# Kernel optimization log

Hardware: AMD Instinct MI355X
Metric: run time of the kernel (lower is better)

Reference implementation:

```python
import jax, jax.numpy as jnp
import numpy as np

N = 100000      # nodes
E = 3200000     # edges (avg degree 32)
F_IN = 128      # data.num_features
H = 64          # hidden_channels
L = 64          # num_layers
C = 47          # data.num_classes
ALPHA = 0.1
THETA = 0.5


def setup_inputs() -> dict:
    key = jax.random.key(0)
    ks = jax.random.split(key, 8)
    x = jax.random.normal(ks[0], (N, F_IN), dtype=jnp.float32)
    edge_index = jax.random.randint(ks[1], (2, E), 0, N, dtype=jnp.int64)
    # Linear(F_IN, H), Linear(H, C), and L shared GCN2Conv weights [H, H]
    W1 = jax.random.normal(ks[2], (F_IN, H), dtype=jnp.float32) * 0.05
    b1 = jnp.zeros((H,), dtype=jnp.float32)
    conv_W = jax.random.normal(ks[3], (L, H, H), dtype=jnp.float32) * 0.05
    W2 = jax.random.normal(ks[4], (H, C), dtype=jnp.float32) * 0.05
    b2 = jnp.zeros((C,), dtype=jnp.float32)
    return {"x": x, "edge_index": edge_index, "W1": W1, "b1": b1,
            "conv_W": conv_W, "W2": W2, "b2": b2}


def reference(x, edge_index, W1, b1, conv_W, W2, b2):
    # --- normalized adjacency with renormalization trick: D^-1/2 (A + I) D^-1/2, transposed ---
    sl = jnp.arange(N, dtype=edge_index.dtype)
    r = jnp.concatenate([edge_index[1], sl])  # adj_t rows (destinations)
    c = jnp.concatenate([edge_index[0], sl])  # adj_t cols (sources)
    deg = jax.ops.segment_sum(jnp.ones((r.shape[0],), jnp.float32), r, num_segments=N)
    dinv = jax.lax.rsqrt(deg)                 # self-loops guarantee deg >= 1
    w = dinv[r] * dinv[c]                     # [E + N] edge weights

    def spmm(h):  # A_hat @ h via gather + segment scatter-add
        return jax.ops.segment_sum(w[:, None] * h[c], r, num_segments=N)

    # dropout is identity in eval mode
    x0 = jax.nn.relu(x @ W1 + b1)             # [N, H]
    betas = jnp.log(THETA / jnp.arange(1, L + 1, dtype=jnp.float32) + 1.0)

    def step(h, layer):
        Wl, beta = layer
        p = spmm(h)
        s = (1.0 - ALPHA) * p + ALPHA * x0    # initial-residual mix
        h = jax.nn.relu((1.0 - beta) * s + beta * (s @ Wl))  # identity mapping
        return h, None

    h, _ = jax.lax.scan(step, x0, (conv_W, betas))
    logits = h @ W2 + b2                      # [N, C]
    return jax.nn.log_softmax(logits, axis=-1)
```

## Files before the change

### kernel.cpp

```cpp
#include <hip/hip_runtime.h>
#include <hip/hip_bf16.h>
#include <math.h>

#define NN 100000
#define NE 3200000
#define FIN 128
#define HD 64
#define NL 64
#define NC 47
#define RPW 4
#define WPB 4
#define RPB (RPW * WPB)

#define SEGSH 13
#define NSEG 13
#define NKEY (NN * NSEG)
#define KB ((NKEY + 1023) / 1024)


__device__ __forceinline__ float bf2f(unsigned short u) {
    union { unsigned int i; float f; } v; v.i = ((unsigned int)u) << 16; return v.f;
}
__device__ __forceinline__ unsigned short f2bf(float f) {
    __hip_bfloat16 h = __float2bfloat16(f);
    return *reinterpret_cast<unsigned short*>(&h);
}
__device__ __forceinline__ float bflo(unsigned int u) {
    union { unsigned int i; float f; } v; v.i = u << 16; return v.f;
}
__device__ __forceinline__ float bfhi(unsigned int u) {
    union { unsigned int i; float f; } v; v.i = u & 0xFFFF0000u; return v.f;
}
__device__ __forceinline__ float fin_at(const void* p, int isf32, size_t i) {
    return isf32 ? ((const float*)p)[i]
                 : __bfloat162float(((const __hip_bfloat16*)p)[i]);
}
__device__ __forceinline__ int edge_at(const void* p, int is64, size_t i) {
    return is64 ? (int)((const long long*)p)[i] : ((const int*)p)[i];
}


__global__ void detect_kernel(const void* __restrict__ x, const void* __restrict__ eidx,
                              int* __restrict__ flags) {
    if (threadIdx.x == 0 && blockIdx.x == 0) {
        const unsigned short* u = (const unsigned short*)x;
        int sane = 0;
        for (int i = 0; i < 64; i++) {
            unsigned short v = u[2 * i];
            int e = (v >> 7) & 0xFF;
            if ((v & 0x7FFF) == 0 || (e >= 90 && e <= 141)) sane++;
        }
        flags[0] = (sane >= 48) ? 0 : 1;
        const int* e32 = (const int*)eidx;
        int nz = 0;
        for (int i = 0; i < 64; i++) if (e32[2 * i + 1] != 0) nz++;
        flags[1] = (nz == 0) ? 1 : 0;
    }
}


__global__ void key_count(const void* __restrict__ eidx, const int* __restrict__ flags,
                          int* __restrict__ cnt) {
    int e = blockIdx.x * blockDim.x + threadIdx.x;
    if (e < NE) {
        int is64 = flags[1];
        int s = edge_at(eidx, is64, (size_t)e);
        int d = edge_at(eidx, is64, (size_t)NE + e);
        atomicAdd(&cnt[d * NSEG + (s >> SEGSH)], 1);
    }
}

__global__ __launch_bounds__(1024) void scan_reduce(const int* __restrict__ cnt,
                                                    int* __restrict__ bsum) {
    __shared__ int lds[1024];
    int tid = threadIdx.x;
    int i = blockIdx.x * 1024 + tid;
    lds[tid] = (i < NKEY) ? cnt[i] : 0;
    __syncthreads();
    for (int off = 512; off > 0; off >>= 1) {
        if (tid < off) lds[tid] += lds[tid + off];
        __syncthreads();
    }
    if (tid == 0) bsum[blockIdx.x] = lds[0];
}

__global__ __launch_bounds__(1024) void scan_mid(int* __restrict__ bsum, int* __restrict__ total_out) {
    __shared__ int lds[1024];
    __shared__ int base_s;
    int tid = threadIdx.x;
    if (tid == 0) base_s = 0;
    __syncthreads();
    for (int chunk = 0; chunk < KB; chunk += 1024) {
        int i = chunk + tid;
        int v = (i < KB) ? bsum[i] : 0;
        lds[tid] = v;
        __syncthreads();
        for (int off = 1; off < 1024; off <<= 1) {
            int t = (tid >= off) ? lds[tid - off] : 0;
            __syncthreads();
            lds[tid] += t;
            __syncthreads();
        }
        int incl = lds[tid];
        int base = base_s;
        if (i < KB) bsum[i] = base + incl - v;
        __syncthreads();
        if (tid == 1023) base_s = base + incl;
        __syncthreads();
    }
    if (tid == 0) *total_out = base_s;
}

__global__ __launch_bounds__(1024) void scan_final(const int* __restrict__ cnt,
                                                   const int* __restrict__ bsum,
                                                   int* __restrict__ keyptr) {
    __shared__ int lds[1024];
    int tid = threadIdx.x;
    int i = blockIdx.x * 1024 + tid;
    int v = (i < NKEY) ? cnt[i] : 0;
    lds[tid] = v;
    __syncthreads();
    for (int off = 1; off < 1024; off <<= 1) {
        int t = (tid >= off) ? lds[tid - off] : 0;
        __syncthreads();
        lds[tid] += t;
        __syncthreads();
    }
    if (i < NKEY) keyptr[i] = bsum[blockIdx.x] + lds[tid] - v;
}

__global__ void dinv_kernel(const int* __restrict__ keyptr, float* __restrict__ dinv) {
    int i = blockIdx.x * blockDim.x + threadIdx.x;
    if (i < NN) {
        int deg = keyptr[(i + 1) * NSEG] - keyptr[i * NSEG];
        dinv[i] = rsqrtf(1.0f + (float)deg);
    }
}

__global__ void scatter_kernel(const void* __restrict__ eidx, const int* __restrict__ flags,
                               const int* __restrict__ keyptr, int* __restrict__ fill,
                               int* __restrict__ col) {
    int e = blockIdx.x * blockDim.x + threadIdx.x;
    if (e < NE) {
        int is64 = flags[1];
        int s = edge_at(eidx, is64, (size_t)e);
        int d = edge_at(eidx, is64, (size_t)NE + e);
        int key = d * NSEG + (s >> SEGSH);
        int pos = keyptr[key] + atomicAdd(&fill[key], 1);
        col[pos] = s;
    }
}


__global__ __launch_bounds__(256) void x0_kernel(const void* __restrict__ x,
                                                 const void* __restrict__ W1,
                                                 const void* __restrict__ b1,
                                                 const int* __restrict__ flags,
                                                 const float* __restrict__ dinv,
                                                 unsigned short* __restrict__ x0b,
                                                 unsigned short* __restrict__ g0) {
    __shared__ float lw[FIN * HD];
    int isf = flags[0];
    int tid = threadIdx.x;
    for (int i = tid; i < FIN * HD; i += 256) lw[i] = fin_at(W1, isf, i);
    __syncthreads();
    int wave = tid >> 6, lane = tid & 63;
    int row0 = blockIdx.x * RPB + wave * RPW;
    if (row0 >= NN) return;
    unsigned int pa01, pa23, pb01, pb23;
    {
        unsigned short a0 = f2bf(fin_at(x, isf, (size_t)(row0 + 0) * FIN + lane));
        unsigned short a1 = f2bf(fin_at(x, isf, (size_t)(row0 + 1) * FIN + lane));
        unsigned short a2 = f2bf(fin_at(x, isf, (size_t)(row0 + 2) * FIN + lane));
        unsigned short a3 = f2bf(fin_at(x, isf, (size_t)(row0 + 3) * FIN + lane));
        unsigned short c0 = f2bf(fin_at(x, isf, (size_t)(row0 + 0) * FIN + 64 + lane));
        unsigned short c1 = f2bf(fin_at(x, isf, (size_t)(row0 + 1) * FIN + 64 + lane));
        unsigned short c2 = f2bf(fin_at(x, isf, (size_t)(row0 + 2) * FIN + 64 + lane));
        unsigned short c3 = f2bf(fin_at(x, isf, (size_t)(row0 + 3) * FIN + 64 + lane));
        pa01 = ((unsigned int)a0 << 16) | a1;  pa23 = ((unsigned int)a2 << 16) | a3;
        pb01 = ((unsigned int)c0 << 16) | c1;  pb23 = ((unsigned int)c2 << 16) | c3;
    }
    float bias = fin_at(b1, isf, lane);
    float d0 = bias, d1 = bias, d2 = bias, d3 = bias;
    #pragma unroll 8
    for (int k = 0; k < 64; k++) {
        float w = lw[k * HD + lane];
        unsigned int b01 = __shfl(pa01, k, 64);
        unsigned int b23 = __shfl(pa23, k, 64);
        union { unsigned int i; float f; } f0, f1, f2, f3;
        f0.i = b01 & 0xFFFF0000u; f1.i = b01 << 16;
        f2.i = b23 & 0xFFFF0000u; f3.i = b23 << 16;
        d0 += f0.f * w; d1 += f1.f * w; d2 += f2.f * w; d3 += f3.f * w;
    }
    #pragma unroll 8
    for (int k = 0; k < 64; k++) {
        float w = lw[(64 + k) * HD + lane];
        unsigned int b01 = __shfl(pb01, k, 64);
        unsigned int b23 = __shfl(pb23, k, 64);
        union { unsigned int i; float f; } f0, f1, f2, f3;
        f0.i = b01 & 0xFFFF0000u; f1.i = b01 << 16;
        f2.i = b23 & 0xFFFF0000u; f3.i = b23 << 16;
        d0 += f0.f * w; d1 += f1.f * w; d2 += f2.f * w; d3 += f3.f * w;
    }
    float dd[RPW] = {d0, d1, d2, d3};
    #pragma unroll
    for (int r = 0; r < RPW; r++) {
        int row = row0 + r;
        if (row >= NN) continue;
        float v = fmaxf(dd[r], 0.0f);
        x0b[(size_t)row * HD + lane] = f2bf(v);
        g0[(size_t)row * HD + lane] = f2bf(dinv[row] * v);
    }
}


__global__ __launch_bounds__(256, 8) void layer_fused(const int* __restrict__ keyptr,
                                                      const int* __restrict__ col,
                                                      const float* __restrict__ dinv,
                                                      const unsigned short* __restrict__ g_in,
                                                      const unsigned short* __restrict__ x0b,
                                                      unsigned short* __restrict__ g_out,
                                                      const void* __restrict__ convW, int layer,
                                                      const int* __restrict__ flags, float beta) {
    __shared__ float lw[HD * HD];
    int isf = flags[0];
    size_t wbase = (size_t)layer * HD * HD;
    int tid = threadIdx.x;
    for (int i = tid; i < HD * HD; i += 256) lw[i] = fin_at(convW, isf, wbase + i);
    __syncthreads();

    int wave = __builtin_amdgcn_readfirstlane(tid >> 6);
    int lane = tid & 63;
    int eslot = lane >> 3;
    int sbyte = (lane & 7) << 4;
    const char* gb = (const char*)g_in;

    int row0 = blockIdx.x * RPB + wave * RPW;

    float sacc[RPW];
    float dsc[RPW];
    #pragma unroll
    for (int r = 0; r < RPW; r++) {
        int row = row0 + r;
        if (row >= NN) { sacc[r] = 0.0f; dsc[r] = 1.0f; continue; }
        int start = keyptr[row * NSEG];
        int end   = keyptr[(row + 1) * NSEG];

        float a0 = 0.0f, a1 = 0.0f, a2 = 0.0f, a3 = 0.0f;
        float a4 = 0.0f, a5 = 0.0f, a6 = 0.0f, a7 = 0.0f;

        for (int j = start; j < end; j += 32) {
            int le = end - 1;
            int i0 = j + eslot, i1 = i0 + 8, i2 = i0 + 16, i3 = i0 + 24;
            int c0 = col[i0 < end ? i0 : le];
            int c1 = col[i1 < end ? i1 : le];
            int c2 = col[i2 < end ? i2 : le];
            int c3 = col[i3 < end ? i3 : le];
            uint4 u0 = *reinterpret_cast<const uint4*>(gb + (((size_t)c0) << 7) + sbyte);
            uint4 u1 = *reinterpret_cast<const uint4*>(gb + (((size_t)c1) << 7) + sbyte);
            uint4 u2 = *reinterpret_cast<const uint4*>(gb + (((size_t)c2) << 7) + sbyte);
            uint4 u3 = *reinterpret_cast<const uint4*>(gb + (((size_t)c3) << 7) + sbyte);
            float m0 = (i0 < end) ? 1.0f : 0.0f;
            float m1 = (i1 < end) ? 1.0f : 0.0f;
            float m2 = (i2 < end) ? 1.0f : 0.0f;
            float m3 = (i3 < end) ? 1.0f : 0.0f;
            a0 = fmaf(m0, bflo(u0.x), a0); a1 = fmaf(m0, bfhi(u0.x), a1);
            a2 = fmaf(m0, bflo(u0.y), a2); a3 = fmaf(m0, bfhi(u0.y), a3);
            a4 = fmaf(m0, bflo(u0.z), a4); a5 = fmaf(m0, bfhi(u0.z), a5);
            a6 = fmaf(m0, bflo(u0.w), a6); a7 = fmaf(m0, bfhi(u0.w), a7);
            a0 = fmaf(m1, bflo(u1.x), a0); a1 = fmaf(m1, bfhi(u1.x), a1);
            a2 = fmaf(m1, bflo(u1.y), a2); a3 = fmaf(m1, bfhi(u1.y), a3);
            a4 = fmaf(m1, bflo(u1.z), a4); a5 = fmaf(m1, bfhi(u1.z), a5);
            a6 = fmaf(m1, bflo(u1.w), a6); a7 = fmaf(m1, bfhi(u1.w), a7);
            a0 = fmaf(m2, bflo(u2.x), a0); a1 = fmaf(m2, bfhi(u2.x), a1);
            a2 = fmaf(m2, bflo(u2.y), a2); a3 = fmaf(m2, bfhi(u2.y), a3);
            a4 = fmaf(m2, bflo(u2.z), a4); a5 = fmaf(m2, bfhi(u2.z), a5);
            a6 = fmaf(m2, bflo(u2.w), a6); a7 = fmaf(m2, bfhi(u2.w), a7);
            a0 = fmaf(m3, bflo(u3.x), a0); a1 = fmaf(m3, bfhi(u3.x), a1);
            a2 = fmaf(m3, bflo(u3.y), a2); a3 = fmaf(m3, bfhi(u3.y), a3);
            a4 = fmaf(m3, bflo(u3.z), a4); a5 = fmaf(m3, bfhi(u3.z), a5);
            a6 = fmaf(m3, bflo(u3.w), a6); a7 = fmaf(m3, bfhi(u3.w), a7);
        }

        a0 += __shfl_xor(a0, 8, 64); a0 += __shfl_xor(a0, 16, 64); a0 += __shfl_xor(a0, 32, 64);
        a1 += __shfl_xor(a1, 8, 64); a1 += __shfl_xor(a1, 16, 64); a1 += __shfl_xor(a1, 32, 64);
        a2 += __shfl_xor(a2, 8, 64); a2 += __shfl_xor(a2, 16, 64); a2 += __shfl_xor(a2, 32, 64);
        a3 += __shfl_xor(a3, 8, 64); a3 += __shfl_xor(a3, 16, 64); a3 += __shfl_xor(a3, 32, 64);
        a4 += __shfl_xor(a4, 8, 64); a4 += __shfl_xor(a4, 16, 64); a4 += __shfl_xor(a4, 32, 64);
        a5 += __shfl_xor(a5, 8, 64); a5 += __shfl_xor(a5, 16, 64); a5 += __shfl_xor(a5, 32, 64);
        a6 += __shfl_xor(a6, 8, 64); a6 += __shfl_xor(a6, 16, 64); a6 += __shfl_xor(a6, 32, 64);
        a7 += __shfl_xor(a7, 8, 64); a7 += __shfl_xor(a7, 16, 64); a7 += __shfl_xor(a7, 32, 64);

        int srcl = lane >> 3;
        float t0 = __shfl(a0, srcl, 64);
        float t1 = __shfl(a1, srcl, 64);
        float t2 = __shfl(a2, srcl, 64);
        float t3 = __shfl(a3, srcl, 64);
        float t4 = __shfl(a4, srcl, 64);
        float t5 = __shfl(a5, srcl, 64);
        float t6 = __shfl(a6, srcl, 64);
        float t7 = __shfl(a7, srcl, 64);
        int b0 = lane & 1, b1 = (lane >> 1) & 1, b2 = (lane >> 2) & 1;
        float s01 = b0 ? t1 : t0, s23 = b0 ? t3 : t2;
        float s45 = b0 ? t5 : t4, s67 = b0 ? t7 : t6;
        float sA = b1 ? s23 : s01, sB = b1 ? s67 : s45;
        float gsum = b2 ? sB : sA;

        float a = gsum + bf2f(g_in[((size_t)row << 6) + lane]);
        float di = dinv[row];
        dsc[r] = di;
        sacc[r] = 0.9f * (di * a) + 0.1f * bf2f(x0b[((size_t)row << 6) + lane]);
    }

    unsigned int p01 = ((unsigned int)f2bf(sacc[0]) << 16) | f2bf(sacc[1]);
    unsigned int p23 = ((unsigned int)f2bf(sacc[2]) << 16) | f2bf(sacc[3]);
    float d0 = 0.0f, d1 = 0.0f, d2 = 0.0f, d3 = 0.0f;
    #pragma unroll 8
    for (int k = 0; k < 64; k++) {
        float w = lw[k * HD + lane];
        unsigned int b01 = __shfl(p01, k, 64);
        unsigned int b23 = __shfl(p23, k, 64);
        union { unsigned int i; float f; } f0, f1, f2, f3;
        f0.i = b01 & 0xFFFF0000u; f1.i = b01 << 16;
        f2.i = b23 & 0xFFFF0000u; f3.i = b23 << 16;
        d0 += f0.f * w; d1 += f1.f * w;
        d2 += f2.f * w; d3 += f3.f * w;
    }

    float dd[RPW] = {d0, d1, d2, d3};
    float omb = 1.0f - beta;
    #pragma unroll
    for (int r = 0; r < RPW; r++) {
        int row = row0 + r;
        if (row >= NN) continue;
        float res = omb * sacc[r] + beta * dd[r];
        g_out[((size_t)row << 6) + lane] = f2bf(dsc[r] * fmaxf(res, 0.0f));
    }
}


__global__ __launch_bounds__(256) void out_kernel(const unsigned short* __restrict__ g,
                                                  const float* __restrict__ dinv,
                                                  const void* __restrict__ W2,
                                                  const void* __restrict__ b2,
                                                  const int* __restrict__ flags,
                                                  void* __restrict__ out) {
    __shared__ float lw[HD * 64];
    int isf = flags[0];
    int tid = threadIdx.x;
    for (int i = tid; i < HD * 64; i += 256) {
        int k = i >> 6, j = i & 63;
        lw[i] = (j < NC) ? fin_at(W2, isf, (size_t)k * NC + j) : 0.0f;
    }
    __syncthreads();
    int row = blockIdx.x * 4 + (tid >> 6);
    int lane = tid & 63;
    if (row >= NN) return;
    float hv = bf2f(g[(size_t)row * HD + lane]) / dinv[row];
    float acc = (lane < NC) ? fin_at(b2, isf, lane) : 0.0f;
    #pragma unroll 8
    for (int k = 0; k < 64; k++) {
        float hk = __shfl(hv, k, 64);
        acc += hk * lw[k * 64 + lane];
    }
    float mv = (lane < NC) ? acc : -1e30f;
    for (int off = 32; off > 0; off >>= 1) mv = fmaxf(mv, __shfl_xor(mv, off, 64));
    float ex = (lane < NC) ? expf(acc - mv) : 0.0f;
    float se = ex;
    for (int off = 32; off > 0; off >>= 1) se += __shfl_xor(se, off, 64);
    float res = acc - mv - logf(se);
    if (lane < NC) {
        size_t oi = (size_t)row * NC + lane;
        if (isf) ((float*)out)[oi] = res;
        else     ((__hip_bfloat16*)out)[oi] = __float2bfloat16(res);
    }
}


static inline size_t align256(size_t x) { return (x + 255) & ~(size_t)255; }

extern "C" void kernel_launch(void* const* d_in, const int* in_sizes, int n_in,
                              void* d_out, int out_size, void* d_ws, size_t ws_size,
                              hipStream_t stream) {
    const void* x     = d_in[0];
    const void* eidx  = d_in[1];
    const void* W1    = d_in[2];
    const void* b1    = d_in[3];
    const void* convW = d_in[4];
    const void* W2    = d_in[5];
    const void* b2    = d_in[6];

    char* p = (char*)d_ws;
    size_t off = 0;
    auto alloc = [&](size_t bytes) { void* r = p + off; off += align256(bytes); return r; };
    int*            flags   = (int*)alloc(256);
    int*            cnt     = (int*)alloc((size_t)NKEY * 4);
    int*            fill    = (int*)alloc((size_t)NKEY * 4);
    int*            keyptr  = (int*)alloc((size_t)(NKEY + 1) * 4);
    int*            bsum    = (int*)alloc((size_t)KB * 4);
    float*          dinv    = (float*)alloc((size_t)NN * 4);
    int*            col     = (int*)alloc((size_t)NE * 4);
    unsigned short* x0b     = (unsigned short*)alloc((size_t)NN * HD * 2);
    unsigned short* hA      = (unsigned short*)alloc((size_t)NN * HD * 2);
    unsigned short* hB      = (unsigned short*)alloc((size_t)NN * HD * 2);

    detect_kernel<<<1, 64, 0, stream>>>(x, eidx, flags);

    hipMemsetAsync(cnt, 0, (size_t)NKEY * 4, stream);
    hipMemsetAsync(fill, 0, (size_t)NKEY * 4, stream);
    key_count<<<(NE + 255) / 256, 256, 0, stream>>>(eidx, flags, cnt);
    scan_reduce<<<KB, 1024, 0, stream>>>(cnt, bsum);
    scan_mid<<<1, 1024, 0, stream>>>(bsum, keyptr + NKEY);
    scan_final<<<KB, 1024, 0, stream>>>(cnt, bsum, keyptr);
    dinv_kernel<<<(NN + 255) / 256, 256, 0, stream>>>(keyptr, dinv);
    scatter_kernel<<<(NE + 255) / 256, 256, 0, stream>>>(eidx, flags, keyptr, fill, col);

    int fb = (NN + RPB - 1) / RPB;
    x0_kernel<<<fb, 256, 0, stream>>>(x, W1, b1, flags, dinv, x0b, hA);

    unsigned short* gin = hA;
    unsigned short* gout = hB;
    for (int l = 0; l < NL; l++) {
        float beta = logf(0.5f / (float)(l + 1) + 1.0f);
        layer_fused<<<fb, 256, 0, stream>>>(keyptr, col, dinv, gin, x0b, gout,
                                            convW, l, flags, beta);
        unsigned short* t = gin; gin = gout; gout = t;
    }
    out_kernel<<<(NN + 3) / 4, 256, 0, stream>>>(gin, dinv, W2, b2, flags, (void*)d_out);
}
```

Baseline: 6.611 ms.

## Split SpMM into source-quadrant partial sums plus separate combine kernel

Edges are now bucketed by source index modulo 4, replacing the old 13-segment source-range bucketing, and each layer runs as two kernels. The first computes per-quadrant partial sums into a float workspace using 8-lane groups that each gather one 128-byte row. The second sums the partials, applies the residual mix and the 64x64 weight matmul. The aim is more parallelism and a different gather pattern, at the cost of writing and reading a 4x N x 64 fp32 buffer every layer plus an extra launch per layer. The old fused path remains as a fallback when the workspace is too small.

```diff
diff --git a/kernel.cpp b/kernel.cpp
--- a/kernel.cpp
+++ b/kernel.cpp
@@ -12,10 +12,12 @@
 #define WPB 4
 #define RPB (RPW * WPB)
 
-#define SEGSH 13
-#define NSEG 13
-#define NKEY (NN * NSEG)
+#define NQ 4
+#define NSEG 4
+#define NKEY (NN * NQ)
 #define KB ((NKEY + 1023) / 1024)
+
+typedef float f32x4 __attribute__((ext_vector_type(4)));
 
 
 __device__ __forceinline__ float bf2f(unsigned short u) {
@@ -60,13 +62,15 @@
 
 
 __global__ void key_count(const void* __restrict__ eidx, const int* __restrict__ flags,
-                          int* __restrict__ cnt) {
+                          int* __restrict__ cnt, int big) {
     int e = blockIdx.x * blockDim.x + threadIdx.x;
     if (e < NE) {
         int is64 = flags[1];
         int s = edge_at(eidx, is64, (size_t)e);
         int d = edge_at(eidx, is64, (size_t)NE + e);
-        atomicAdd(&cnt[d * NSEG + (s >> SEGSH)], 1);
+        int q = s & 3;
+        int key = big ? (q * NN + d) : (d * 4 + q);
+        atomicAdd(&cnt[key], 1);
     }
 }
 
@@ -129,23 +133,32 @@
     if (i < NKEY) keyptr[i] = bsum[blockIdx.x] + lds[tid] - v;
 }
 
-__global__ void dinv_kernel(const int* __restrict__ keyptr, float* __restrict__ dinv) {
+__global__ void dinv_kernel(const int* __restrict__ keyptr, float* __restrict__ dinv, int big) {
     int i = blockIdx.x * blockDim.x + threadIdx.x;
     if (i < NN) {
-        int deg = keyptr[(i + 1) * NSEG] - keyptr[i * NSEG];
+        int deg;
+        if (big) {
+            deg = 0;
+            #pragma unroll
+            for (int q = 0; q < NQ; q++)
+                deg += keyptr[q * NN + i + 1] - keyptr[q * NN + i];
+        } else {
+            deg = keyptr[(i + 1) * NSEG] - keyptr[i * NSEG];
+        }
         dinv[i] = rsqrtf(1.0f + (float)deg);
     }
 }
 
 __global__ void scatter_kernel(const void* __restrict__ eidx, const int* __restrict__ flags,
                                const int* __restrict__ keyptr, int* __restrict__ fill,
-                               int* __restrict__ col) {
+                               int* __restrict__ col, int big) {
     int e = blockIdx.x * blockDim.x + threadIdx.x;
     if (e < NE) {
         int is64 = flags[1];
         int s = edge_at(eidx, is64, (size_t)e);
         int d = edge_at(eidx, is64, (size_t)NE + e);
-        int key = d * NSEG + (s >> SEGSH);
+        int q = s & 3;
+        int key = big ? (q * NN + d) : (d * 4 + q);
         int pos = keyptr[key] + atomicAdd(&fill[key], 1);
         col[pos] = s;
     }
@@ -210,6 +223,111 @@
         float v = fmaxf(dd[r], 0.0f);
         x0b[(size_t)row * HD + lane] = f2bf(v);
         g0[(size_t)row * HD + lane] = f2bf(dinv[row] * v);
+    }
+}
+
+
+__global__ __launch_bounds__(256, 8) void spmm_partial(const int* __restrict__ keyptr,
+                                                       const int* __restrict__ colq,
+                                                       const unsigned short* __restrict__ g_in,
+                                                       float* __restrict__ part) {
+    int bid = blockIdx.x;
+    int quad = bid & 3;
+    int tile = bid >> 2;
+    int tid = threadIdx.x;
+    int wave = tid >> 6, lane = tid & 63;
+    int grp = lane >> 3, li = lane & 7;
+    int row = tile * 32 + wave * 8 + grp;
+    size_t kbase = (size_t)quad * NN + row;
+    int jbeg = keyptr[kbase];
+    int jend = keyptr[kbase + 1];
+    int cnt = jend - jbeg;
+    const char* gb = (const char*)g_in;
+
+    float a0 = 0.0f, a1 = 0.0f, a2 = 0.0f, a3 = 0.0f;
+    float a4 = 0.0f, a5 = 0.0f, a6 = 0.0f, a7 = 0.0f;
+
+    for (int base = 0; base < cnt; base += 8) {
+        int idx = jbeg + base + li;
+        int cv = colq[idx < jend ? idx : (jend - 1)];
+        int rem = cnt - base;
+        #pragma unroll
+        for (int k = 0; k < 8; k++) {
+            if (k < rem) {
+                int ck = __shfl(cv, (lane & 56) + k, 64);
+                uint4 u = *reinterpret_cast<const uint4*>(gb + (((size_t)ck) << 7) + (li << 4));
+                a0 += bflo(u.x); a1 += bfhi(u.x);
+                a2 += bflo(u.y); a3 += bfhi(u.y);
+                a4 += bflo(u.z); a5 += bfhi(u.z);
+                a6 += bflo(u.w); a7 += bfhi(u.w);
+            }
+        }
+    }
+
+    f32x4 v0 = {a0, a1, a2, a3};
+    f32x4 v1 = {a4, a5, a6, a7};
+    float* pp = part + kbase * HD + (li << 3);
+    __builtin_nontemporal_store(v0, reinterpret_cast<f32x4*>(pp));
+    __builtin_nontemporal_store(v1, reinterpret_cast<f32x4*>(pp + 4));
+}
+
+
+__global__ __launch_bounds__(256, 8) void layer_combine(const float* __restrict__ part,
+                                                        const float* __restrict__ dinv,
+                                                        const unsigned short* __restrict__ g_in,
+                                                        const unsigned short* __restrict__ x0b,
+                                                        unsigned short* __restrict__ g_out,
+                                                        const void* __restrict__ convW, int layer,
+                                                        const int* __restrict__ flags, float beta) {
+    __shared__ float lw[HD * HD];
+    int isf = flags[0];
+    size_t wbase = (size_t)layer * HD * HD;
+    int tid = threadIdx.x;
+    for (int i = tid; i < HD * HD; i += 256) lw[i] = fin_at(convW, isf, wbase + i);
+    __syncthreads();
+
+    int wave = __builtin_amdgcn_readfirstlane(tid >> 6);
+    int lane = tid & 63;
+    int row0 = blockIdx.x * RPB + wave * RPW;
+
+    float sacc[RPW];
+    float dsc[RPW];
+    #pragma unroll
+    for (int r = 0; r < RPW; r++) {
+        int row = row0 + r;
+        if (row >= NN) { sacc[r] = 0.0f; dsc[r] = 1.0f; continue; }
+        float a = bf2f(g_in[((size_t)row << 6) + lane]);
+        #pragma unroll
+        for (int q = 0; q < NQ; q++)
+            a += __builtin_nontemporal_load(part + ((size_t)q * NN + row) * HD + lane);
+        float di = dinv[row];
+        dsc[r] = di;
+        sacc[r] = 0.9f * (di * a) + 0.1f * bf2f(x0b[((size_t)row << 6) + lane]);
+    }
+
+    unsigned int p01 = ((unsigned int)f2bf(sacc[0]) << 16) | f2bf(sacc[1]);
+    unsigned int p23 = ((unsigned int)f2bf(sacc[2]) << 16) | f2bf(sacc[3]);
+    float d0 = 0.0f, d1 = 0.0f, d2 = 0.0f, d3 = 0.0f;
+    #pragma unroll 8
+    for (int k = 0; k < 64; k++) {
+        float w = lw[k * HD + lane];
+        unsigned int b01 = __shfl(p01, k, 64);
+        unsigned int b23 = __shfl(p23, k, 64);
+        union { unsigned int i; float f; } f0, f1, f2, f3;
+        f0.i = b01 & 0xFFFF0000u; f1.i = b01 << 16;
+        f2.i = b23 & 0xFFFF0000u; f3.i = b23 << 16;
+        d0 += f0.f * w; d1 += f1.f * w;
+        d2 += f2.f * w; d3 += f3.f * w;
+    }
+
+    float dd[RPW] = {d0, d1, d2, d3};
+    float omb = 1.0f - beta;
+    #pragma unroll
+    for (int r = 0; r < RPW; r++) {
+        int row = row0 + r;
+        if (row >= NN) continue;
+        float res = omb * sacc[r] + beta * dd[r];
+        g_out[((size_t)row << 6) + lane] = f2bf(dsc[r] * fmaxf(res, 0.0f));
     }
 }
 
@@ -404,16 +522,20 @@
     unsigned short* hA      = (unsigned short*)alloc((size_t)NN * HD * 2);
     unsigned short* hB      = (unsigned short*)alloc((size_t)NN * HD * 2);
 
+    size_t part_bytes = (size_t)NQ * NN * HD * 4;
+    int big = (off + part_bytes) <= ws_size;
+    float* part = (float*)(p + off);
+
     detect_kernel<<<1, 64, 0, stream>>>(x, eidx, flags);
 
     hipMemsetAsync(cnt, 0, (size_t)NKEY * 4, stream);
     hipMemsetAsync(fill, 0, (size_t)NKEY * 4, stream);
-    key_count<<<(NE + 255) / 256, 256, 0, stream>>>(eidx, flags, cnt);
+    key_count<<<(NE + 255) / 256, 256, 0, stream>>>(eidx, flags, cnt, big);
     scan_reduce<<<KB, 1024, 0, stream>>>(cnt, bsum);
     scan_mid<<<1, 1024, 0, stream>>>(bsum, keyptr + NKEY);
     scan_final<<<KB, 1024, 0, stream>>>(cnt, bsum, keyptr);
-    dinv_kernel<<<(NN + 255) / 256, 256, 0, stream>>>(keyptr, dinv);
-    scatter_kernel<<<(NE + 255) / 256, 256, 0, stream>>>(eidx, flags, keyptr, fill, col);
+    dinv_kernel<<<(NN + 255) / 256, 256, 0, stream>>>(keyptr, dinv, big);
+    scatter_kernel<<<(NE + 255) / 256, 256, 0, stream>>>(eidx, flags, keyptr, fill, col, big);
 
     int fb = (NN + RPB - 1) / RPB;
     x0_kernel<<<fb, 256, 0, stream>>>(x, W1, b1, flags, dinv, x0b, hA);
@@ -422,8 +544,14 @@
     unsigned short* gout = hB;
     for (int l = 0; l < NL; l++) {
         float beta = logf(0.5f / (float)(l + 1) + 1.0f);
-        layer_fused<<<fb, 256, 0, stream>>>(keyptr, col, dinv, gin, x0b, gout,
-                                            convW, l, flags, beta);
+        if (big) {
+            spmm_partial<<<(NN / 32) * NQ, 256, 0, stream>>>(keyptr, col, gin, part);
+            layer_combine<<<fb, 256, 0, stream>>>(part, dinv, gin, x0b, gout,
+                                                  convW, l, flags, beta);
+        } else {
+            layer_fused<<<fb, 256, 0, stream>>>(keyptr, col, dinv, gin, x0b, gout,
+                                                convW, l, flags, beta);
+        }
         unsigned short* t = gin; gin = gout; gout = t;
     }
     out_kernel<<<(NN + 3) / 4, 256, 0, stream>>>(gin, dinv, W2, b2, flags, (void*)d_out);
```

Result: slower. 7.449 ms (+12.7%).
